# Performance work log

Hardware: AMD Instinct MI355X
Metric: run time of the kernel (lower is better)

## Reference

```python
import jax, jax.numpy as jnp
import numpy as np

B, N, FD, HD, G = 32, 512, 768, 384, 3
ALPHA = 0.2  # LeakyReLU slope
NEG = -9e15


def layer_norm(x, g, b, eps=1e-5):
    m = jnp.mean(x, axis=-1, keepdims=True)
    v = jnp.var(x, axis=-1, keepdims=True)
    return (x - m) / jnp.sqrt(v + eps) * g + b


def gat_layer(x, adj, W, a):
    # x: [B,N,FD], adj: [N,N], W: [FD,HD], a: [2*HD]
    h = jnp.einsum('bnf,fd->bnd', x, W)  # [B,N,HD]
    # concat score decomposes: e_ij = lrelu(h_i . a[:HD] + h_j . a[HD:])
    e1 = h @ a[:HD]   # [B,N]
    e2 = h @ a[HD:]   # [B,N]
    e = jax.nn.leaky_relu(e1[:, :, None] + e2[:, None, :], ALPHA)  # [B,N,N]
    e = jnp.where(adj[None] > 0, e, NEG)
    att = jax.nn.softmax(e, axis=2)  # masked softmax over neighbors
    h_prime = jnp.einsum('bij,bjd->bid', att, h)
    return jax.nn.elu(h_prime)  # concat=True -> ELU


def setup_inputs() -> dict:
    key = jax.random.key(0)
    ks = jax.random.split(key, 10)
    s = 0.05
    return {
        'x': jax.random.normal(ks[0], (B, N, FD), jnp.float32),
        'adj': jax.random.randint(ks[1], (G, N, N), 0, 2),
        'W': jax.random.normal(ks[2], (G, FD, HD), jnp.float32) * s,
        'a': jax.random.normal(ks[3], (G, 2 * HD), jnp.float32) * s,
        'log_unc': jnp.zeros((G,), jnp.float32),
        'gate_w': jax.random.normal(ks[4], (FD, G), jnp.float32) * s,
        'gate_b': jnp.zeros((G,), jnp.float32),
        'ln1_g': jnp.ones((HD,), jnp.float32),
        'ln1_b': jnp.zeros((HD,), jnp.float32),
        'w1': jax.random.normal(ks[5], (HD, HD), jnp.float32) * s,
        'b1': jnp.zeros((HD,), jnp.float32),
        'w2': jax.random.normal(ks[6], (HD, FD), jnp.float32) * s,
        'b2': jnp.zeros((FD,), jnp.float32),
        'ln2_g': jnp.ones((FD,), jnp.float32),
        'ln2_b': jnp.zeros((FD,), jnp.float32),
    }


def reference(x, adj, W, a, log_unc, gate_w, gate_b, ln1_g, ln1_b,
              w1, b1, w2, b2, ln2_g, ln2_b):
    # global (uncertainty) weights
    unc = jnp.exp(log_unc)
    attw = jax.nn.softmax(1.0 / (unc + 1e-8))  # [G]
    # content gates from batch-averaged features
    avg = jnp.mean(x, axis=0)                          # [N,FD]
    cg = jax.nn.softmax(avg @ gate_w + gate_b, axis=-1)  # [N,G]
    # per-graph GAT + LayerNorm, vmapped over the G graphs
    gouts = jax.vmap(lambda ad, Wi, ai: layer_norm(gat_layer(x, ad, Wi, ai), ln1_g, ln1_b))(adj, W, a)  # [G,B,N,HD]
    weights = 0.7 * attw[:, None, None, None] + 0.3 * cg.T[:, None, :, None]  # [G,1|B,N,1]
    fused = jnp.sum(weights * gouts, axis=0)  # [B,N,HD]
    # output projection + LayerNorm
    proj = jax.nn.relu(fused @ w1 + b1) @ w2 + b2
    proj = layer_norm(proj, ln2_g, ln2_b)
    # residual gate
    gv = jax.nn.sigmoid(jnp.sum(proj * x, axis=-1, keepdims=True) / np.sqrt(FD).astype(np.float32))
    return gv * x + (1.0 - gv) * proj
```

## Files before the change

kernel.cpp:

```cpp
#include <hip/hip_runtime.h>

typedef unsigned short ushort_t;
typedef unsigned int uint_t;
typedef __bf16 bf16x8 __attribute__((ext_vector_type(8)));
typedef float f32x4 __attribute__((ext_vector_type(4)));
typedef unsigned int u32x4 __attribute__((ext_vector_type(4)));
typedef unsigned short u16x4 __attribute__((ext_vector_type(4)));
typedef unsigned short u16x8 __attribute__((ext_vector_type(8)));

#define B_SZ 32
#define N_SZ 512
#define FD_SZ 768
#define HD_SZ 384
#define G_SZ 3
#define M_SZ (B_SZ * N_SZ)
#define ALPHA_LR 0.2f
#define NEGV -9.0e15f
#define VTILE (HD_SZ * 32)
#define PSLICE ((size_t)M_SZ * HD_SZ)

__device__ __forceinline__ float bf2f(ushort_t u) { return __uint_as_float(((uint_t)u) << 16); }
__device__ __forceinline__ ushort_t f2bf(float f) {
  uint_t x = __float_as_uint(f);
  return (ushort_t)((x + 0x7fffu + ((x >> 16) & 1u)) >> 16);
}
__device__ __forceinline__ u32x4 pack8(f32x4 lo, f32x4 hi) {
  union { ushort_t us[8]; u32x4 v; } pk;
  pk.us[0] = f2bf(lo.x); pk.us[1] = f2bf(lo.y); pk.us[2] = f2bf(lo.z); pk.us[3] = f2bf(lo.w);
  pk.us[4] = f2bf(hi.x); pk.us[5] = f2bf(hi.y); pk.us[6] = f2bf(hi.z); pk.us[7] = f2bf(hi.w);
  return pk.v;
}

__global__ __launch_bounds__(256) void transpose_f2b(
    const float* __restrict__ src, ushort_t* __restrict__ dst, int R, int C) {
  size_t total = (size_t)R * C;
  size_t base = (size_t)blockIdx.z * total;
  size_t i = (size_t)blockIdx.x * 256 + threadIdx.x;
  if (i < total) {
    int r = (int)(i / C), c = (int)(i % C);
    dst[base + (size_t)c * R + r] = f2bf(src[base + i]);
  }
}

__global__ __launch_bounds__(256) void cast_f2b(
    const float* __restrict__ src, ushort_t* __restrict__ dst) {
  size_t i = (size_t)blockIdx.x * 256 + threadIdx.x;
  f32x4 v = ((const f32x4*)src)[i];
  u16x4 p;
  p[0] = f2bf(v.x); p[1] = f2bf(v.y); p[2] = f2bf(v.z); p[3] = f2bf(v.w);
  ((u16x4*)dst)[i] = p;
}

__global__ __launch_bounds__(256) void pack_adj(
    const int* __restrict__ adj, uint_t* __restrict__ am) {
  size_t i = (size_t)blockIdx.x * 256 + threadIdx.x;
  unsigned long long mask = __ballot(adj[i] != 0);
  int lane = threadIdx.x & 63;
  if ((lane & 31) == 0) am[i >> 5] = (uint_t)(mask >> (lane & 32));
}

__global__ __launch_bounds__(256) void gate_kernel(
    const float* __restrict__ x, const float* __restrict__ gate_w,
    const float* __restrict__ gate_b, float* __restrict__ cg) {
  int n = blockIdx.x;
  int tid = threadIdx.x;
  float a0 = 0.f, a1 = 0.f, a2 = 0.f;
  for (int f = tid; f < FD_SZ; f += 256) {
    float s = 0.f;
#pragma unroll
    for (int b = 0; b < B_SZ; b++) s += x[((size_t)b * N_SZ + n) * FD_SZ + f];
    float avg = s * (1.0f / B_SZ);
    a0 += avg * gate_w[f * 3 + 0];
    a1 += avg * gate_w[f * 3 + 1];
    a2 += avg * gate_w[f * 3 + 2];
  }
  for (int m = 1; m < 64; m <<= 1) {
    a0 += __shfl_xor(a0, m, 64);
    a1 += __shfl_xor(a1, m, 64);
    a2 += __shfl_xor(a2, m, 64);
  }
  __shared__ float red[3][4];
  int wave = tid >> 6, lane = tid & 63;
  if (lane == 0) { red[0][wave] = a0; red[1][wave] = a1; red[2][wave] = a2; }
  __syncthreads();
  if (tid == 0) {
    float l0 = red[0][0] + red[0][1] + red[0][2] + red[0][3] + gate_b[0];
    float l1 = red[1][0] + red[1][1] + red[1][2] + red[1][3] + gate_b[1];
    float l2 = red[2][0] + red[2][1] + red[2][2] + red[2][3] + gate_b[2];
    float mx = fmaxf(l0, fmaxf(l1, l2));
    float e0 = __expf(l0 - mx), e1 = __expf(l1 - mx), e2 = __expf(l2 - mx);
    float inv = 1.0f / (e0 + e1 + e2);
    cg[n * 3 + 0] = e0 * inv;
    cg[n * 3 + 1] = e1 * inv;
    cg[n * 3 + 2] = e2 * inv;
  }
}

template <bool AF32, bool RELU, bool OUTBF16, bool HASBIAS, bool VFOUT>
__global__ __launch_bounds__(256) void gemm_kernel(
    const void* __restrict__ Av, size_t strideA,
    const ushort_t* __restrict__ Bt, size_t strideB,
    const float* __restrict__ bias,
    void* __restrict__ Cv, size_t strideC,
    int M, int K, int Nc) {
  __shared__ __attribute__((aligned(16))) ushort_t As[128 * 32];
  __shared__ __attribute__((aligned(16))) ushort_t Bs[128 * 32];
  int tid = threadIdx.x, wave = tid >> 6, lane = tid & 63;
  int m0 = blockIdx.y * 128, n0 = blockIdx.x * 128;
  const float* Abf32 = (const float*)Av + (size_t)blockIdx.z * strideA;
  const ushort_t* Abb16 = (const ushort_t*)Av + (size_t)blockIdx.z * strideA;
  const ushort_t* Bb = Bt + (size_t)blockIdx.z * strideB;

  f32x4 acc[4][4];
  f32x4 z4 = {0.f, 0.f, 0.f, 0.f};
#pragma unroll
  for (int i = 0; i < 4; i++)
#pragma unroll
    for (int j = 0; j < 4; j++) acc[i][j] = z4;

  int wm = (wave & 1) * 64, wn = (wave >> 1) * 64;
  int srow = lane >> 2, schk = (lane & 3) * 8;

  for (int kt = 0; kt < K; kt += 32) {
    u32x4 av[2], bv[2];
#pragma unroll
    for (int i = 0; i < 2; i++) {
      int row = m0 + wave * 32 + i * 16 + srow;
      if (AF32) {
        const float* ap = Abf32 + (size_t)row * K + kt + schk;
        f32x4 lo = *(const f32x4*)ap;
        f32x4 hi = *(const f32x4*)(ap + 4);
        av[i] = pack8(lo, hi);
      } else {
        av[i] = *(const u32x4*)(Abb16 + (size_t)row * K + kt + schk);
      }
      bv[i] = *(const u32x4*)(Bb + (size_t)(n0 + wave * 32 + i * 16 + srow) * K + kt + schk);
    }
    __syncthreads();
#pragma unroll
    for (int i = 0; i < 2; i++) {
      int rowBase = wave * 32 + i * 16;
      *(u32x4*)(As + rowBase * 32 + lane * 8) = av[i];
      *(u32x4*)(Bs + rowBase * 32 + lane * 8) = bv[i];
    }
    __syncthreads();
    bf16x8 af[4], bfr[4];
#pragma unroll
    for (int t = 0; t < 4; t++) {
      af[t] = *(const bf16x8*)(As + (wm + t * 16 + (lane & 15)) * 32 + (lane >> 4) * 8);
      bfr[t] = *(const bf16x8*)(Bs + (wn + t * 16 + (lane & 15)) * 32 + (lane >> 4) * 8);
    }
#pragma unroll
    for (int mt = 0; mt < 4; mt++)
#pragma unroll
      for (int nt = 0; nt < 4; nt++)
        acc[mt][nt] = __builtin_amdgcn_mfma_f32_16x16x32_bf16(af[mt], bfr[nt], acc[mt][nt], 0, 0, 0);
  }

  if (VFOUT) {
#pragma unroll
    for (int mt = 0; mt < 4; mt++) {
#pragma unroll
      for (int nt = 0; nt < 4; nt++) {
        int d = n0 + wn + nt * 16 + (lane & 15);
        int gm = m0 + wm + mt * 16 + (lane >> 4) * 4;
        int b = gm >> 9, jt = (gm >> 5) & 15, j2 = gm & 31;
        u16x4 pk;
#pragma unroll
        for (int r2 = 0; r2 < 4; r2++) pk[r2] = f2bf(acc[mt][nt][r2]);
        size_t off = ((size_t)((blockIdx.z * B_SZ + b) * 16 + jt)) * VTILE + (size_t)d * 32 + j2;
        *(u16x4*)((ushort_t*)Cv + off) = pk;
      }
    }
  } else {
#pragma unroll
    for (int mt = 0; mt < 4; mt++) {
#pragma unroll
      for (int nt = 0; nt < 4; nt++) {
        int gn = n0 + wn + nt * 16 + (lane & 15);
        float bvs = HASBIAS ? bias[gn] : 0.f;
#pragma unroll
        for (int r2 = 0; r2 < 4; r2++) {
          int gm = m0 + wm + mt * 16 + (lane >> 4) * 4 + r2;
          float v = acc[mt][nt][r2] + bvs;
          if (RELU) v = v > 0.f ? v : 0.f;
          size_t off = (size_t)blockIdx.z * strideC + (size_t)gm * Nc + gn;
          if (OUTBF16) ((ushort_t*)Cv)[off] = f2bf(v);
          else ((float*)Cv)[off] = v;
        }
      }
    }
  }
}

__global__ __launch_bounds__(256) void e12_kernel(
    const ushort_t* __restrict__ vf, const float* __restrict__ a,
    float* __restrict__ e1, float* __restrict__ e2) {
  __shared__ float a1s[HD_SZ], a2s[HD_SZ];
  int g = blockIdx.y;
  int tid = threadIdx.x;
  for (int i = tid; i < HD_SZ; i += 256) {
    a1s[i] = a[g * 2 * HD_SZ + i];
    a2s[i] = a[g * 2 * HD_SZ + HD_SZ + i];
  }
  __syncthreads();
  int m = blockIdx.x * 256 + tid;
  int b = m >> 9, jt = (m >> 5) & 15, j2 = m & 31;
  const ushort_t* col = vf + ((size_t)((g * B_SZ + b) * 16 + jt)) * VTILE + j2;
  float s1 = 0.f, s2 = 0.f;
  for (int d = 0; d < HD_SZ; d++) {
    float h = bf2f(col[d * 32]);
    s1 += h * a1s[d];
    s2 += h * a2s[d];
  }
  e1[(size_t)g * M_SZ + m] = s1;
  e2[(size_t)g * M_SZ + m] = s2;
}

__global__ __launch_bounds__(512, 4) void attn_kernel(
    const uint_t* __restrict__ adjm, const ushort_t* __restrict__ vf,
    const float* __restrict__ e1, const float* __restrict__ e2,
    const float* __restrict__ cg, const float* __restrict__ log_unc,
    const float* __restrict__ ln1g, const float* __restrict__ ln1b,
    ushort_t* __restrict__ pf) {
  __shared__ __attribute__((aligned(16))) ushort_t Pb[32][520];
  __shared__ float e2s[512];
  __shared__ float e1r[32];
  __shared__ uint_t amS[32][16];
  __shared__ float lng[HD_SZ], lnb[HD_SZ];
  __shared__ float cgr[32];
  __shared__ float s1s[32][8], s2s[32][8];

  int tid = threadIdx.x, wave = tid >> 6, lane = tid & 63;
  int quad = lane >> 4, l15 = lane & 15;
  int g = blockIdx.z;
  int L = blockIdx.x + (blockIdx.y << 4);
  int b = (L & 7) + ((L >> 7) << 3);
  int i0 = ((L >> 3) & 15) * 32;

  float iv0 = 1.f / (__expf(log_unc[0]) + 1e-8f);
  float iv1 = 1.f / (__expf(log_unc[1]) + 1e-8f);
  float iv2 = 1.f / (__expf(log_unc[2]) + 1e-8f);
  float mxa = fmaxf(iv0, fmaxf(iv1, iv2));
  float w0 = __expf(iv0 - mxa), w1 = __expf(iv1 - mxa), w2 = __expf(iv2 - mxa);
  float wsum = 1.f / (w0 + w1 + w2);
  float attwg = (g == 0 ? w0 : (g == 1 ? w1 : w2)) * wsum;

  if (tid < HD_SZ) {
    lng[tid] = ln1g[tid];
    lnb[tid] = ln1b[tid];
  }
  if (tid < 32) {
    cgr[tid] = cg[(i0 + tid) * 3 + g];
    e1r[tid] = e1[((size_t)g * B_SZ + b) * N_SZ + i0 + tid];
  }
  amS[tid >> 4][tid & 15] = adjm[((size_t)g * N_SZ + i0 + (tid >> 4)) * 16 + (tid & 15)];
  e2s[tid] = e2[((size_t)g * B_SZ + b) * N_SZ + tid];
  __syncthreads();

#pragma unroll
  for (int rr = 0; rr < 4; rr++) {
    int rw = wave * 4 + rr;
    float e1v = e1r[rw];
    float sv[8];
    float m = -3.0e38f;
#pragma unroll
    for (int jj = 0; jj < 8; jj++) {
      int j = lane + jj * 64;
      float s = e1v + e2s[j];
      s = s > 0.f ? s : ALPHA_LR * s;
      uint_t mw = amS[rw][(lane >> 5) + jj * 2];
      s = ((mw >> (j & 31)) & 1u) ? s : NEGV;
      sv[jj] = s;
      m = fmaxf(m, s);
    }
    for (int msk = 1; msk < 64; msk <<= 1) m = fmaxf(m, __shfl_xor(m, msk, 64));
    float sum = 0.f;
#pragma unroll
    for (int jj = 0; jj < 8; jj++) {
      float e = __expf(sv[jj] - m);
      sv[jj] = e;
      sum += e;
    }
    for (int msk = 1; msk < 64; msk <<= 1) sum += __shfl_xor(sum, msk, 64);
    float inv = 1.0f / sum;
#pragma unroll
    for (int jj = 0; jj < 8; jj++) Pb[rw][lane + jj * 64] = f2bf(sv[jj] * inv);
  }
  __syncthreads();

  f32x4 acc[2][3];
  f32x4 z4 = {0.f, 0.f, 0.f, 0.f};
#pragma unroll
  for (int mt = 0; mt < 2; mt++)
#pragma unroll
    for (int t = 0; t < 3; t++) acc[mt][t] = z4;
  const ushort_t* vbase = vf + ((size_t)(g * B_SZ + b) * 16) * VTILE;
#pragma unroll 2
  for (int j0 = 0; j0 < N_SZ; j0 += 32) {
    const ushort_t* vtile = vbase + (size_t)(j0 >> 5) * VTILE;
    bf16x8 af0 = *(const bf16x8*)(&Pb[l15][j0 + quad * 8]);
    bf16x8 af1 = *(const bf16x8*)(&Pb[16 + l15][j0 + quad * 8]);
#pragma unroll
    for (int t = 0; t < 3; t++) {
      bf16x8 bf = *(const bf16x8*)(vtile + (wave * 48 + t * 16 + l15) * 32 + quad * 8);
      acc[0][t] = __builtin_amdgcn_mfma_f32_16x16x32_bf16(af0, bf, acc[0][t], 0, 0, 0);
      acc[1][t] = __builtin_amdgcn_mfma_f32_16x16x32_bf16(af1, bf, acc[1][t], 0, 0, 0);
    }
  }

  float ps1[2][4], ps2[2][4];
#pragma unroll
  for (int mt = 0; mt < 2; mt++)
#pragma unroll
    for (int r = 0; r < 4; r++) { ps1[mt][r] = 0.f; ps2[mt][r] = 0.f; }
#pragma unroll
  for (int mt = 0; mt < 2; mt++)
#pragma unroll
    for (int t = 0; t < 3; t++)
#pragma unroll
      for (int r = 0; r < 4; r++) {
        float v = acc[mt][t][r];
        v = v > 0.f ? v : __expf(v) - 1.f;
        acc[mt][t][r] = v;
        ps1[mt][r] += v;
        ps2[mt][r] += v * v;
      }
#pragma unroll
  for (int msk = 1; msk < 16; msk <<= 1) {
#pragma unroll
    for (int mt = 0; mt < 2; mt++)
#pragma unroll
      for (int r = 0; r < 4; r++) {
        ps1[mt][r] += __shfl_xor(ps1[mt][r], msk, 64);
        ps2[mt][r] += __shfl_xor(ps2[mt][r], msk, 64);
      }
  }
  if (l15 == 0) {
#pragma unroll
    for (int mt = 0; mt < 2; mt++)
#pragma unroll
      for (int r = 0; r < 4; r++) {
        s1s[mt * 16 + quad * 4 + r][wave] = ps1[mt][r];
        s2s[mt * 16 + quad * 4 + r][wave] = ps2[mt][r];
      }
  }
  __syncthreads();
#pragma unroll
  for (int mt = 0; mt < 2; mt++)
#pragma unroll
    for (int r = 0; r < 4; r++) {
      int row = mt * 16 + quad * 4 + r;
      float S1 = 0.f, S2 = 0.f;
#pragma unroll
      for (int w = 0; w < 8; w++) {
        S1 += s1s[row][w];
        S2 += s2s[row][w];
      }
      float mean = S1 * (1.f / HD_SZ);
      float var = S2 * (1.f / HD_SZ) - mean * mean;
      float rs = rsqrtf(var + 1e-5f);
      float wgt = 0.7f * attwg + 0.3f * cgr[row];
      size_t rowo = (size_t)g * PSLICE + ((size_t)b * N_SZ + i0 + row) * HD_SZ;
#pragma unroll
      for (int t = 0; t < 3; t++) {
        int d = wave * 48 + t * 16 + l15;
        pf[rowo + d] = f2bf(wgt * ((acc[mt][t][r] - mean) * rs * lng[d] + lnb[d]));
      }
    }
}

__global__ __launch_bounds__(256) void reduce3_kernel(
    const ushort_t* __restrict__ pf, ushort_t* __restrict__ fused) {
  size_t u = ((size_t)blockIdx.x * 256 + threadIdx.x) * 8;
  u16x8 a = *(const u16x8*)(pf + u);
  u16x8 b = *(const u16x8*)(pf + PSLICE + u);
  u16x8 c = *(const u16x8*)(pf + 2 * PSLICE + u);
  u16x8 o;
#pragma unroll
  for (int k = 0; k < 8; k++)
    o[k] = f2bf(bf2f(a[k]) + bf2f(b[k]) + bf2f(c[k]));
  *(u16x8*)(fused + u) = o;
}

__global__ __launch_bounds__(256) void final_kernel(
    const ushort_t* __restrict__ projbf, const float* __restrict__ x,
    const float* __restrict__ ln2g, const float* __restrict__ ln2b,
    float* __restrict__ out) {
  int row = blockIdx.x;
  int tid = threadIdx.x, wave = tid >> 6, lane = tid & 63;
  const ushort_t* pr = projbf + (size_t)row * FD_SZ;
  const float* xr = x + (size_t)row * FD_SZ;
  float v[3], xv[3];
  float s1 = 0.f, s2 = 0.f;
#pragma unroll
  for (int k = 0; k < 3; k++) {
    int c = tid + k * 256;
    v[k] = bf2f(pr[c]);
    xv[k] = xr[c];
    s1 += v[k];
    s2 += v[k] * v[k];
  }
  for (int m = 1; m < 64; m <<= 1) {
    s1 += __shfl_xor(s1, m, 64);
    s2 += __shfl_xor(s2, m, 64);
  }
  __shared__ float rs1[4], rs2[4], rdt[4];
  if (lane == 0) { rs1[wave] = s1; rs2[wave] = s2; }
  __syncthreads();
  s1 = rs1[0] + rs1[1] + rs1[2] + rs1[3];
  s2 = rs2[0] + rs2[1] + rs2[2] + rs2[3];
  float mean = s1 * (1.f / FD_SZ);
  float var = s2 * (1.f / FD_SZ) - mean * mean;
  float rstd = rsqrtf(var + 1e-5f);
  float dot = 0.f;
  float pn[3];
#pragma unroll
  for (int k = 0; k < 3; k++) {
    int c = tid + k * 256;
    pn[k] = (v[k] - mean) * rstd * ln2g[c] + ln2b[c];
    dot += pn[k] * xv[k];
  }
  for (int m = 1; m < 64; m <<= 1) dot += __shfl_xor(dot, m, 64);
  if (lane == 0) rdt[wave] = dot;
  __syncthreads();
  dot = rdt[0] + rdt[1] + rdt[2] + rdt[3];
  float gv = 1.f / (1.f + __expf(-dot * (1.0f / 27.712812921102035f)));
#pragma unroll
  for (int k = 0; k < 3; k++) {
    int c = tid + k * 256;
    out[(size_t)row * FD_SZ + c] = gv * xv[k] + (1.f - gv) * pn[k];
  }
}

extern "C" void kernel_launch(void* const* d_in, const int* in_sizes, int n_in,
                              void* d_out, int out_size, void* d_ws, size_t ws_size,
                              hipStream_t stream) {
  (void)in_sizes; (void)n_in; (void)out_size; (void)ws_size;
  const float* x = (const float*)d_in[0];
  const int* adj = (const int*)d_in[1];
  const float* W = (const float*)d_in[2];
  const float* a = (const float*)d_in[3];
  const float* log_unc = (const float*)d_in[4];
  const float* gate_w = (const float*)d_in[5];
  const float* gate_b = (const float*)d_in[6];
  const float* ln1g = (const float*)d_in[7];
  const float* ln1b = (const float*)d_in[8];
  const float* w1 = (const float*)d_in[9];
  const float* b1 = (const float*)d_in[10];
  const float* w2 = (const float*)d_in[11];
  const float* b2 = (const float*)d_in[12];
  const float* ln2g = (const float*)d_in[13];
  const float* ln2b = (const float*)d_in[14];

  char* ws = (char*)d_ws;
  ushort_t* Wt      = (ushort_t*)(ws + 0);
  uint_t*   adjm    = (uint_t*)(ws + 0);
  ushort_t* w1t     = (ushort_t*)(ws + 1769472);
  ushort_t* w2t     = (ushort_t*)(ws + 2064384);
  float*    cg      = (float*)(ws + 2654208);
  float*    e1      = (float*)(ws + 2660352);
  float*    e2      = (float*)(ws + 2856960);
  ushort_t* fusedbf = (ushort_t*)(ws + 3053568);
  ushort_t* vf      = (ushort_t*)(ws + 15636480);
  ushort_t* t1bf    = (ushort_t*)(ws + 15636480);
  ushort_t* projbf  = (ushort_t*)(ws + 28219392);
  ushort_t* xb      = (ushort_t*)d_out;
  ushort_t* pf      = (ushort_t*)d_out;

  cast_f2b<<<dim3((M_SZ * FD_SZ) / 1024), 256, 0, stream>>>(x, xb);

  transpose_f2b<<<dim3(1152, 1, 3), 256, 0, stream>>>(W, Wt, FD_SZ, HD_SZ);
  transpose_f2b<<<dim3(576, 1, 1), 256, 0, stream>>>(w1, w1t, HD_SZ, HD_SZ);
  transpose_f2b<<<dim3(1152, 1, 1), 256, 0, stream>>>(w2, w2t, HD_SZ, FD_SZ);

  gate_kernel<<<dim3(N_SZ), 256, 0, stream>>>(x, gate_w, gate_b, cg);

  gemm_kernel<false, false, true, false, true><<<dim3(3, 128, 3), 256, 0, stream>>>(
      xb, 0, Wt, (size_t)HD_SZ * FD_SZ, nullptr, vf, 0,
      M_SZ, FD_SZ, HD_SZ);

  pack_adj<<<dim3((G_SZ * N_SZ * N_SZ) / 256), 256, 0, stream>>>(adj, adjm);

  e12_kernel<<<dim3(M_SZ / 256, G_SZ), 256, 0, stream>>>(vf, a, e1, e2);

  attn_kernel<<<dim3(N_SZ / 32, B_SZ, G_SZ), 512, 0, stream>>>(
      adjm, vf, e1, e2, cg, log_unc, ln1g, ln1b, pf);

  reduce3_kernel<<<dim3((M_SZ * HD_SZ) / (256 * 8)), 256, 0, stream>>>(pf, fusedbf);

  gemm_kernel<false, true, true, true, false><<<dim3(3, 128, 1), 256, 0, stream>>>(
      fusedbf, 0, w1t, 0, b1, t1bf, 0, M_SZ, HD_SZ, HD_SZ);
  gemm_kernel<false, false, true, true, false><<<dim3(6, 128, 1), 256, 0, stream>>>(
      t1bf, 0, w2t, 0, b2, projbf, 0, M_SZ, HD_SZ, FD_SZ);

  final_kernel<<<dim3(M_SZ), 256, 0, stream>>>(projbf, x, ln2g, ln2b, (float*)d_out);
}
```

Baseline: 341.2 us.

## Load GEMM tiles directly into LDS, split e12 reduction, prioritize attn MFMA

The GEMM kernel now copies A and B tiles straight from global memory into LDS with global_load_lds instead of staging them in registers, and the unused fp32-A path is removed. The e12 kernel splits each 384-length dot product across four threads and combines them with shuffles, giving four times as many blocks and shorter serial loops. The attention kernel raises wave priority around its MFMA loop. The direct-to-LDS loads skip register staging, but they still sit between barriers with no prefetch, so memory latency stays exposed.

```diff
diff --git a/kernel.cpp b/kernel.cpp
--- a/kernel.cpp
+++ b/kernel.cpp
@@ -24,11 +24,11 @@
   uint_t x = __float_as_uint(f);
   return (ushort_t)((x + 0x7fffu + ((x >> 16) & 1u)) >> 16);
 }
-__device__ __forceinline__ u32x4 pack8(f32x4 lo, f32x4 hi) {
-  union { ushort_t us[8]; u32x4 v; } pk;
-  pk.us[0] = f2bf(lo.x); pk.us[1] = f2bf(lo.y); pk.us[2] = f2bf(lo.z); pk.us[3] = f2bf(lo.w);
-  pk.us[4] = f2bf(hi.x); pk.us[5] = f2bf(hi.y); pk.us[6] = f2bf(hi.z); pk.us[7] = f2bf(hi.w);
-  return pk.v;
+
+__device__ __forceinline__ void gload_lds16(const ushort_t* g, ushort_t* l) {
+  __builtin_amdgcn_global_load_lds(
+      (const __attribute__((address_space(1))) uint_t*)(const void*)g,
+      (__attribute__((address_space(3))) uint_t*)(void*)l, 16, 0, 0);
 }
 
 __global__ __launch_bounds__(256) void transpose_f2b(
@@ -96,9 +96,9 @@
   }
 }
 
-template <bool AF32, bool RELU, bool OUTBF16, bool HASBIAS, bool VFOUT>
+template <bool RELU, bool OUTBF16, bool HASBIAS, bool VFOUT>
 __global__ __launch_bounds__(256) void gemm_kernel(
-    const void* __restrict__ Av, size_t strideA,
+    const ushort_t* __restrict__ Ab, size_t strideA,
     const ushort_t* __restrict__ Bt, size_t strideB,
     const float* __restrict__ bias,
     void* __restrict__ Cv, size_t strideC,
@@ -107,8 +107,7 @@
   __shared__ __attribute__((aligned(16))) ushort_t Bs[128 * 32];
   int tid = threadIdx.x, wave = tid >> 6, lane = tid & 63;
   int m0 = blockIdx.y * 128, n0 = blockIdx.x * 128;
-  const float* Abf32 = (const float*)Av + (size_t)blockIdx.z * strideA;
-  const ushort_t* Abb16 = (const ushort_t*)Av + (size_t)blockIdx.z * strideA;
+  const ushort_t* A = Ab + (size_t)blockIdx.z * strideA;
   const ushort_t* Bb = Bt + (size_t)blockIdx.z * strideB;
 
   f32x4 acc[4][4];
@@ -122,26 +121,14 @@
   int srow = lane >> 2, schk = (lane & 3) * 8;
 
   for (int kt = 0; kt < K; kt += 32) {
-    u32x4 av[2], bv[2];
-#pragma unroll
-    for (int i = 0; i < 2; i++) {
-      int row = m0 + wave * 32 + i * 16 + srow;
-      if (AF32) {
-        const float* ap = Abf32 + (size_t)row * K + kt + schk;
-        f32x4 lo = *(const f32x4*)ap;
-        f32x4 hi = *(const f32x4*)(ap + 4);
-        av[i] = pack8(lo, hi);
-      } else {
-        av[i] = *(const u32x4*)(Abb16 + (size_t)row * K + kt + schk);
-      }
-      bv[i] = *(const u32x4*)(Bb + (size_t)(n0 + wave * 32 + i * 16 + srow) * K + kt + schk);
-    }
     __syncthreads();
 #pragma unroll
     for (int i = 0; i < 2; i++) {
       int rowBase = wave * 32 + i * 16;
-      *(u32x4*)(As + rowBase * 32 + lane * 8) = av[i];
-      *(u32x4*)(Bs + rowBase * 32 + lane * 8) = bv[i];
+      gload_lds16(A + (size_t)(m0 + rowBase + srow) * K + kt + schk,
+                  As + rowBase * 32);
+      gload_lds16(Bb + (size_t)(n0 + rowBase + srow) * K + kt + schk,
+                  Bs + rowBase * 32);
     }
     __syncthreads();
     bf16x8 af[4], bfr[4];
@@ -204,17 +191,23 @@
     a2s[i] = a[g * 2 * HD_SZ + HD_SZ + i];
   }
   __syncthreads();
-  int m = blockIdx.x * 256 + tid;
+  int m = blockIdx.x * 64 + (tid >> 2), dq = tid & 3;
   int b = m >> 9, jt = (m >> 5) & 15, j2 = m & 31;
   const ushort_t* col = vf + ((size_t)((g * B_SZ + b) * 16 + jt)) * VTILE + j2;
   float s1 = 0.f, s2 = 0.f;
-  for (int d = 0; d < HD_SZ; d++) {
+#pragma unroll 4
+  for (int k = 0; k < 96; k++) {
+    int d = dq * 96 + k;
     float h = bf2f(col[d * 32]);
     s1 += h * a1s[d];
     s2 += h * a2s[d];
   }
-  e1[(size_t)g * M_SZ + m] = s1;
-  e2[(size_t)g * M_SZ + m] = s2;
+  s1 += __shfl_xor(s1, 1, 64); s1 += __shfl_xor(s1, 2, 64);
+  s2 += __shfl_xor(s2, 1, 64); s2 += __shfl_xor(s2, 2, 64);
+  if (dq == 0) {
+    e1[(size_t)g * M_SZ + m] = s1;
+    e2[(size_t)g * M_SZ + m] = s2;
+  }
 }
 
 __global__ __launch_bounds__(512, 4) void attn_kernel(
@@ -296,6 +289,7 @@
 #pragma unroll
     for (int t = 0; t < 3; t++) acc[mt][t] = z4;
   const ushort_t* vbase = vf + ((size_t)(g * B_SZ + b) * 16) * VTILE;
+  __builtin_amdgcn_s_setprio(1);
 #pragma unroll 2
   for (int j0 = 0; j0 < N_SZ; j0 += 32) {
     const ushort_t* vtile = vbase + (size_t)(j0 >> 5) * VTILE;
@@ -308,6 +302,7 @@
       acc[1][t] = __builtin_amdgcn_mfma_f32_16x16x32_bf16(af1, bf, acc[1][t], 0, 0, 0);
     }
   }
+  __builtin_amdgcn_s_setprio(0);
 
   float ps1[2][4], ps2[2][4];
 #pragma unroll
@@ -476,22 +471,22 @@
 
   gate_kernel<<<dim3(N_SZ), 256, 0, stream>>>(x, gate_w, gate_b, cg);
 
-  gemm_kernel<false, false, true, false, true><<<dim3(3, 128, 3), 256, 0, stream>>>(
+  gemm_kernel<false, true, false, true><<<dim3(3, 128, 3), 256, 0, stream>>>(
       xb, 0, Wt, (size_t)HD_SZ * FD_SZ, nullptr, vf, 0,
       M_SZ, FD_SZ, HD_SZ);
 
   pack_adj<<<dim3((G_SZ * N_SZ * N_SZ) / 256), 256, 0, stream>>>(adj, adjm);
 
-  e12_kernel<<<dim3(M_SZ / 256, G_SZ), 256, 0, stream>>>(vf, a, e1, e2);
+  e12_kernel<<<dim3(M_SZ / 64, G_SZ), 256, 0, stream>>>(vf, a, e1, e2);
 
   attn_kernel<<<dim3(N_SZ / 32, B_SZ, G_SZ), 512, 0, stream>>>(
       adjm, vf, e1, e2, cg, log_unc, ln1g, ln1b, pf);
 
   reduce3_kernel<<<dim3((M_SZ * HD_SZ) / (256 * 8)), 256, 0, stream>>>(pf, fusedbf);
 
-  gemm_kernel<false, true, true, true, false><<<dim3(3, 128, 1), 256, 0, stream>>>(
+  gemm_kernel<true, true, true, false><<<dim3(3, 128, 1), 256, 0, stream>>>(
       fusedbf, 0, w1t, 0, b1, t1bf, 0, M_SZ, HD_SZ, HD_SZ);
-  gemm_kernel<false, false, true, true, false><<<dim3(6, 128, 1), 256, 0, stream>>>(
+  gemm_kernel<false, true, true, false><<<dim3(6, 128, 1), 256, 0, stream>>>(
       t1bf, 0, w2t, 0, b2, projbf, 0, M_SZ, HD_SZ, FD_SZ);
 
   final_kernel<<<dim3(M_SZ), 256, 0, stream>>>(projbf, x, ln2g, ln2b, (float*)d_out);
```

Result: no change. 335.9 us (-1.6%).
